# Kernel optimization log

Hardware: AMD Instinct MI355X
Metric: run time of the kernel (lower is better)

The kernel has to match this reference:

```python
import jax, jax.numpy as jnp
import numpy as np

B, T, L = 512, 1024, 48


def setup_inputs() -> dict:
    key = jax.random.key(0)
    k_e, k_tr, k_st, k_en = jax.random.split(key, 4)
    emissions = jax.random.normal(k_e, (B, T, L), dtype=jnp.float32)
    mask = jnp.ones((B, T), dtype=bool)  # unused by the original decode body
    transitions = jax.random.normal(k_tr, (L, L), dtype=jnp.float32) * 0.1
    start_transitions = jax.random.normal(k_st, (L,), dtype=jnp.float32) * 0.1
    end_transitions = jax.random.normal(k_en, (L,), dtype=jnp.float32) * 0.1
    return {
        "emissions": emissions,
        "mask": mask,
        "transitions": transitions,
        "start_transitions": start_transitions,
        "end_transitions": end_transitions,
    }


def reference(emissions, mask, transitions, start_transitions, end_transitions):
    # Viterbi forward (max-plus recurrence) over time, vectorized over batch.
    v0 = start_transitions[None, :] + emissions[:, 0]  # [B, L]

    def step(v, e_t):
        # scores[b, i, j] = v[b, i] + transitions[i, j]
        scores = v[:, :, None] + transitions[None, :, :]  # [B, L, L]
        best = jnp.max(scores, axis=1)                    # [B, L]
        bp = jnp.argmax(scores, axis=1).astype(jnp.int32)  # [B, L] best prev tag
        return best + e_t, bp

    em_rest = jnp.moveaxis(emissions[:, 1:], 1, 0)  # [T-1, B, L]
    v_final, bps = jax.lax.scan(step, v0, em_rest)  # bps: [T-1, B, L]
    v_final = v_final + end_transitions[None, :]
    best_last = jnp.argmax(v_final, axis=1).astype(jnp.int32)  # [B]

    # Backtrack: bps[t] maps tag at time t+1 -> best tag at time t.
    def back(tag, bp):
        prev = jnp.take_along_axis(bp, tag[:, None], axis=1)[:, 0]  # [B]
        return prev, prev

    _, tags_0_to_Tm2 = jax.lax.scan(back, best_last, bps, reverse=True)  # [T-1, B]
    paths = jnp.concatenate([tags_0_to_Tm2, best_last[None, :]], axis=0)  # [T, B]
    return paths.T  # [B, T] decoded tag sequences
```

## Files before the change

kernel.cpp:

```cpp
#include <hip/hip_runtime.h>
#include <math.h>

#define BB 512
#define TT 1024
#define LL 48

__device__ __forceinline__ float readlane_f(float v, int lane) {
    return __int_as_float(__builtin_amdgcn_readlane(__float_as_int(v), lane));
}

__device__ __forceinline__ void argmax48(const float* s, float& bestv, int& besti) {
    float val[24];
    int   idx[24];
#pragma unroll
    for (int k = 0; k < 24; ++k) {
        bool c = s[2 * k + 1] > s[2 * k];
        val[k] = c ? s[2 * k + 1] : s[2 * k];
        idx[k] = c ? 2 * k + 1 : 2 * k;
    }
#pragma unroll
    for (int k = 0; k < 12; ++k) {
        bool c = val[2 * k + 1] > val[2 * k];
        val[k] = c ? val[2 * k + 1] : val[2 * k];
        idx[k] = c ? idx[2 * k + 1] : idx[2 * k];
    }
#pragma unroll
    for (int k = 0; k < 6; ++k) {
        bool c = val[2 * k + 1] > val[2 * k];
        val[k] = c ? val[2 * k + 1] : val[2 * k];
        idx[k] = c ? idx[2 * k + 1] : idx[2 * k];
    }
#pragma unroll
    for (int k = 0; k < 3; ++k) {
        bool c = val[2 * k + 1] > val[2 * k];
        val[k] = c ? val[2 * k + 1] : val[2 * k];
        idx[k] = c ? idx[2 * k + 1] : idx[2 * k];
    }
    bool c01 = val[1] > val[0];
    float bv = c01 ? val[1] : val[0];
    int   bi = c01 ? idx[1] : idx[0];
    bool c2 = val[2] > bv;
    bestv = c2 ? val[2] : bv;
    besti = c2 ? idx[2] : bi;
}

__global__ __launch_bounds__(64) void viterbi_kernel(
    const float* __restrict__ emissions,
    const float* __restrict__ transitions,
    const float* __restrict__ start_tr,
    const float* __restrict__ end_tr,
    int* __restrict__ out)
{
    __shared__ unsigned char bp[(TT - 1) * LL];

    const int b = blockIdx.x;
    const int j = threadIdx.x;
    const int jc = (j < LL) ? j : (LL - 1);

    float tc[LL];
#pragma unroll
    for (int i = 0; i < LL; ++i)
        tc[i] = transitions[i * LL + jc];

    const float* em = emissions + (size_t)b * TT * LL;

    float v = start_tr[jc] + em[jc];

    float e1 = em[1 * LL + jc];
    float e2 = em[2 * LL + jc];

#pragma unroll 3
    for (int t = 1; t < TT; ++t) {
        int tn = t + 2; if (tn >= TT) tn = TT - 1;
        float e3 = em[(size_t)tn * LL + jc];

        float s[LL];
#pragma unroll
        for (int i = 0; i < LL; ++i)
            s[i] = readlane_f(v, i) + tc[i];

        float best; int arg;
        argmax48(s, best, arg);

        v = best + e1;
        bp[(t - 1) * LL + jc] = (unsigned char)arg;

        e1 = e2; e2 = e3;
    }

    v += end_tr[jc];

    float sf[LL];
#pragma unroll
    for (int i = 0; i < LL; ++i)
        sf[i] = readlane_f(v, i);

    float bestv; int tag;
    argmax48(sf, bestv, tag);

    int* ob = out + (size_t)b * TT;
    if (j == 0) ob[TT - 1] = tag;

    __syncthreads();

    for (int hi = TT - 2; hi >= 0; hi -= 32) {
        int lo = hi - 31; if (lo < 0) lo = 0;
        int n = hi - lo + 1;

        unsigned int row[32];
#pragma unroll
        for (int k = 0; k < 32; ++k)
            row[k] = (unsigned int)bp[(lo + k) * LL + jc];

        int outv = 0;
#pragma unroll
        for (int k = 31; k >= 0; --k) {
            if (k < n) {
                tag = __builtin_amdgcn_readlane((int)row[k], tag);
                outv = (j == k) ? tag : outv;
            }
        }
        if (j < n) ob[lo + j] = outv;
    }
}

extern "C" void kernel_launch(void* const* d_in, const int* in_sizes, int n_in,
                              void* d_out, int out_size, void* d_ws, size_t ws_size,
                              hipStream_t stream) {
    const float* emissions   = (const float*)d_in[0];
    const float* transitions = (const float*)d_in[2];
    const float* start_tr    = (const float*)d_in[3];
    const float* end_tr      = (const float*)d_in[4];
    int* out = (int*)d_out;

    viterbi_kernel<<<dim3(BB), dim3(64), 0, stream>>>(
        emissions, transitions, start_tr, end_tr, out);
}
```

Before: 582.4 us.

## Split the Viterbi max-plus reduction across four wavefronts with LDS combine

Each block now runs four wavefronts instead of one. Each wavefront computes a partial max/argmax over 12 of the 48 previous tags. The partial results are packed as value/index pairs into a double-buffered LDS array, and every wave then merges the four candidates after a block barrier. The goal is to cut the serial readlane-and-compare chain per timestep, which dominates this latency-bound recurrence. The cost is an LDS round trip and a __syncthreads on every step, plus four times as many threads holding redundant state. Only wave 0 writes backpointers and runs the backtrack.

```diff
diff --git a/kernel.cpp b/kernel.cpp
--- a/kernel.cpp
+++ b/kernel.cpp
@@ -4,6 +4,8 @@
 #define BB 512
 #define TT 1024
 #define LL 48
+#define NW 4
+#define IW 12
 
 __device__ __forceinline__ float readlane_f(float v, int lane) {
     return __int_as_float(__builtin_amdgcn_readlane(__float_as_int(v), lane));
@@ -44,7 +46,7 @@
     besti = c2 ? idx[2] : bi;
 }
 
-__global__ __launch_bounds__(64) void viterbi_kernel(
+__global__ __launch_bounds__(256) void viterbi_kernel(
     const float* __restrict__ emissions,
     const float* __restrict__ transitions,
     const float* __restrict__ start_tr,
@@ -52,15 +54,19 @@
     int* __restrict__ out)
 {
     __shared__ unsigned char bp[(TT - 1) * LL];
+    __shared__ unsigned long long cb[2][NW * LL];
 
-    const int b = blockIdx.x;
-    const int j = threadIdx.x;
-    const int jc = (j < LL) ? j : (LL - 1);
+    const int b   = blockIdx.x;
+    const int tid = threadIdx.x;
+    const int w   = tid >> 6;
+    const int j   = tid & 63;
+    const int jc  = (j < LL) ? j : (LL - 1);
+    const int ibase = w * IW;
 
-    float tc[LL];
+    float tc[IW];
 #pragma unroll
-    for (int i = 0; i < LL; ++i)
-        tc[i] = transitions[i * LL + jc];
+    for (int k = 0; k < IW; ++k)
+        tc[k] = transitions[(ibase + k) * LL + jc];
 
     const float* em = emissions + (size_t)b * TT * LL;
 
@@ -74,19 +80,62 @@
         int tn = t + 2; if (tn >= TT) tn = TT - 1;
         float e3 = em[(size_t)tn * LL + jc];
 
-        float s[LL];
+        float s[IW];
 #pragma unroll
-        for (int i = 0; i < LL; ++i)
-            s[i] = readlane_f(v, i) + tc[i];
+        for (int k = 0; k < IW; ++k)
+            s[k] = readlane_f(v, ibase + k) + tc[k];
 
-        float best; int arg;
-        argmax48(s, best, arg);
+        float val[6]; int idx[6];
+#pragma unroll
+        for (int k = 0; k < 6; ++k) {
+            bool c = s[2 * k + 1] > s[2 * k];
+            val[k] = c ? s[2 * k + 1] : s[2 * k];
+            idx[k] = ibase + (c ? 2 * k + 1 : 2 * k);
+        }
+#pragma unroll
+        for (int k = 0; k < 3; ++k) {
+            bool c = val[2 * k + 1] > val[2 * k];
+            val[k] = c ? val[2 * k + 1] : val[2 * k];
+            idx[k] = c ? idx[2 * k + 1] : idx[2 * k];
+        }
+        bool c01 = val[1] > val[0];
+        float pv = c01 ? val[1] : val[0];
+        int   pa = c01 ? idx[1] : idx[0];
+        bool c2 = val[2] > pv;
+        pv = c2 ? val[2] : pv;
+        pa = c2 ? idx[2] : pa;
+
+        const int p = t & 1;
+        cb[p][w * LL + jc] =
+            ((unsigned long long)(unsigned)pa << 32) | (unsigned)__float_as_uint(pv);
+
+        __syncthreads();
+
+        float V0, V1, V2, V3; int A0, A1, A2, A3;
+        {
+            unsigned long long q0 = cb[p][0 * LL + jc];
+            unsigned long long q1 = cb[p][1 * LL + jc];
+            unsigned long long q2 = cb[p][2 * LL + jc];
+            unsigned long long q3 = cb[p][3 * LL + jc];
+            V0 = __uint_as_float((unsigned)q0); A0 = (int)(q0 >> 32);
+            V1 = __uint_as_float((unsigned)q1); A1 = (int)(q1 >> 32);
+            V2 = __uint_as_float((unsigned)q2); A2 = (int)(q2 >> 32);
+            V3 = __uint_as_float((unsigned)q3); A3 = (int)(q3 >> 32);
+        }
+        bool ca = V1 > V0;  float va = ca ? V1 : V0;  int aa = ca ? A1 : A0;
+        bool cbb = V3 > V2; float vb = cbb ? V3 : V2; int ab = cbb ? A3 : A2;
+        bool cf = vb > va;
+        float best = cf ? vb : va;
+        int   arg  = cf ? ab : aa;
 
         v = best + e1;
-        bp[(t - 1) * LL + jc] = (unsigned char)arg;
+        if (w == 0)
+            bp[(t - 1) * LL + jc] = (unsigned char)arg;
 
         e1 = e2; e2 = e3;
     }
+
+    if (w != 0) return;
 
     v += end_tr[jc];
 
@@ -100,8 +149,6 @@
 
     int* ob = out + (size_t)b * TT;
     if (j == 0) ob[TT - 1] = tag;
-
-    __syncthreads();
 
     for (int hi = TT - 2; hi >= 0; hi -= 32) {
         int lo = hi - 31; if (lo < 0) lo = 0;
@@ -133,6 +180,6 @@
     const float* end_tr      = (const float*)d_in[4];
     int* out = (int*)d_out;
 
-    viterbi_kernel<<<dim3(BB), dim3(64), 0, stream>>>(
+    viterbi_kernel<<<dim3(BB), dim3(256), 0, stream>>>(
         emissions, transitions, start_tr, end_tr, out);
 }
```

Result: slower. 708.5 us (+21.7%).

## Split Viterbi into max-only producer wave and argmax consumer wave

Applied to the files above, without the earlier changes.

The block grows to two wavefronts. Wave 0 runs the serial recurrence using only fmax reductions, which are cheaper than a tracked argmax. It publishes v and best per step into a 32-slot LDS ring. Wave 1 recovers the argmax by equality matching against best, then writes backpointers and does the backtrack, synchronising through volatile LDS counters with s_sleep spin-waits. This takes the index tracking off the latency-critical recurrence, at the cost of LDS traffic, spin-wait overhead, and the risk of ties or ordering issues in the hand-rolled synchronisation.

```diff
diff --git a/kernel.cpp b/kernel.cpp
--- a/kernel.cpp
+++ b/kernel.cpp
@@ -4,9 +4,17 @@
 #define BB 512
 #define TT 1024
 #define LL 48
+#define DD 32
 
 __device__ __forceinline__ float readlane_f(float v, int lane) {
     return __int_as_float(__builtin_amdgcn_readlane(__float_as_int(v), lane));
+}
+
+__device__ __forceinline__ void lds_fence() {
+    asm volatile("s_waitcnt lgkmcnt(0)" ::: "memory");
+}
+__device__ __forceinline__ void nap() {
+    asm volatile("s_sleep 1");
 }
 
 __device__ __forceinline__ void argmax48(const float* s, float& bestv, int& besti) {
@@ -44,7 +52,7 @@
     besti = c2 ? idx[2] : bi;
 }
 
-__global__ __launch_bounds__(64) void viterbi_kernel(
+__global__ __launch_bounds__(128) void viterbi_kernel(
     const float* __restrict__ emissions,
     const float* __restrict__ transitions,
     const float* __restrict__ start_tr,
@@ -52,75 +60,144 @@
     int* __restrict__ out)
 {
     __shared__ unsigned char bp[(TT - 1) * LL];
-
-    const int b = blockIdx.x;
-    const int j = threadIdx.x;
-    const int jc = (j < LL) ? j : (LL - 1);
+    __shared__ __align__(16) float vring[DD][LL];
+    __shared__ __align__(16) float bring[DD][LL];
+    __shared__ int a_cnt, b_cnt, tag_word;
+
+    const int b   = blockIdx.x;
+    const int tid = threadIdx.x;
+    const int w   = tid >> 6;
+    const int j   = tid & 63;
+    const int jc  = (j < LL) ? j : (LL - 1);
+
+    if (tid == 0) { a_cnt = 0; b_cnt = 0; }
+    __syncthreads();
+
+    volatile int* pa = &a_cnt;
+    volatile int* pb = &b_cnt;
 
     float tc[LL];
 #pragma unroll
     for (int i = 0; i < LL; ++i)
         tc[i] = transitions[i * LL + jc];
 
-    const float* em = emissions + (size_t)b * TT * LL;
-
-    float v = start_tr[jc] + em[jc];
-
-    float e1 = em[1 * LL + jc];
-    float e2 = em[2 * LL + jc];
-
-#pragma unroll 3
-    for (int t = 1; t < TT; ++t) {
-        int tn = t + 2; if (tn >= TT) tn = TT - 1;
-        float e3 = em[(size_t)tn * LL + jc];
-
-        float s[LL];
+    int* ob = out + (size_t)b * TT;
+
+    if (w == 0) {
+        const float* em = emissions + (size_t)b * TT * LL;
+        float v = start_tr[jc] + em[jc];
+        float e1 = em[1 * LL + jc];
+        float e2 = em[2 * LL + jc];
+
+#pragma unroll 2
+        for (int t = 1; t < TT; ++t) {
+            if ((t & 7) == 1) {
+                while (*pb < t - 25) nap();
+            }
+            int tn = t + 2; if (tn >= TT) tn = TT - 1;
+            float e3 = em[(size_t)tn * LL + jc];
+
+            const int slot = t & (DD - 1);
+            *(volatile float*)&vring[slot][jc] = v;
+
+            float s[LL];
+#pragma unroll
+            for (int i = 0; i < LL; ++i)
+                s[i] = readlane_f(v, i) + tc[i];
+
+            float m1[16];
+#pragma unroll
+            for (int k = 0; k < 16; ++k)
+                m1[k] = fmaxf(fmaxf(s[3 * k], s[3 * k + 1]), s[3 * k + 2]);
+            float m2[6];
+#pragma unroll
+            for (int k = 0; k < 5; ++k)
+                m2[k] = fmaxf(fmaxf(m1[3 * k], m1[3 * k + 1]), m1[3 * k + 2]);
+            m2[5] = m1[15];
+            float m3a = fmaxf(fmaxf(m2[0], m2[1]), m2[2]);
+            float m3b = fmaxf(fmaxf(m2[3], m2[4]), m2[5]);
+            float best = fmaxf(m3a, m3b);
+
+            *(volatile float*)&bring[slot][jc] = best;
+            lds_fence();
+            if (j == 0) *pa = t;
+
+            v = best + e1;
+            e1 = e2; e2 = e3;
+        }
+
+        v += end_tr[jc];
+        float sf[LL];
 #pragma unroll
         for (int i = 0; i < LL; ++i)
-            s[i] = readlane_f(v, i) + tc[i];
-
-        float best; int arg;
-        argmax48(s, best, arg);
-
-        v = best + e1;
-        bp[(t - 1) * LL + jc] = (unsigned char)arg;
-
-        e1 = e2; e2 = e3;
-    }
-
-    v += end_tr[jc];
-
-    float sf[LL];
-#pragma unroll
-    for (int i = 0; i < LL; ++i)
-        sf[i] = readlane_f(v, i);
-
-    float bestv; int tag;
-    argmax48(sf, bestv, tag);
-
-    int* ob = out + (size_t)b * TT;
-    if (j == 0) ob[TT - 1] = tag;
-
-    __syncthreads();
-
-    for (int hi = TT - 2; hi >= 0; hi -= 32) {
-        int lo = hi - 31; if (lo < 0) lo = 0;
-        int n = hi - lo + 1;
-
-        unsigned int row[32];
-#pragma unroll
-        for (int k = 0; k < 32; ++k)
-            row[k] = (unsigned int)bp[(lo + k) * LL + jc];
-
-        int outv = 0;
-#pragma unroll
-        for (int k = 31; k >= 0; --k) {
-            if (k < n) {
-                tag = __builtin_amdgcn_readlane((int)row[k], tag);
-                outv = (j == k) ? tag : outv;
-            }
-        }
-        if (j < n) ob[lo + j] = outv;
+            sf[i] = readlane_f(v, i);
+        float bestv; int tag;
+        argmax48(sf, bestv, tag);
+        if (j == 0) {
+            ob[TT - 1] = tag;
+            *(volatile int*)&tag_word = tag;
+        }
+        lds_fence();
+        if (j == 0) *pa = TT;
+    } else {
+        for (int t = 1; t < TT; ++t) {
+            while (*pa < t) nap();
+            lds_fence();
+
+            const int slot = t & (DD - 1);
+            const float4* vp = (const float4*)&vring[slot][0];
+            float vb[LL];
+#pragma unroll
+            for (int k = 0; k < 12; ++k) {
+                float4 q = vp[k];
+                vb[4 * k + 0] = q.x; vb[4 * k + 1] = q.y;
+                vb[4 * k + 2] = q.z; vb[4 * k + 3] = q.w;
+            }
+            float best = bring[slot][jc];
+
+            float s[LL];
+#pragma unroll
+            for (int i = 0; i < LL; ++i)
+                s[i] = vb[i] + tc[i];
+
+            int i0 = 63, i1 = 63, i2 = 63, i3 = 63;
+#pragma unroll
+            for (int k = 11; k >= 0; --k) {
+                if (s[k]      == best) i0 = k;
+                if (s[12 + k] == best) i1 = 12 + k;
+                if (s[24 + k] == best) i2 = 24 + k;
+                if (s[36 + k] == best) i3 = 36 + k;
+            }
+            int arg = min(min(i0, i1), min(i2, i3));
+
+            bp[(t - 1) * LL + jc] = (unsigned char)arg;
+
+            if (((t & 7) == 0) && j == 0) *pb = t;
+        }
+
+        while (*pa < TT) nap();
+        lds_fence();
+        int tag = *(volatile int*)&tag_word;
+
+        for (int hi = TT - 2; hi >= 0; hi -= 32) {
+            int lo = hi - 31; if (lo < 0) lo = 0;
+            int n = hi - lo + 1;
+
+            unsigned int row[32];
+#pragma unroll
+            for (int k = 0; k < 32; ++k)
+                row[k] = (unsigned int)bp[(lo + k) * LL + jc];
+
+            int outv = 0;
+#pragma unroll
+            for (int k = 31; k >= 0; --k) {
+                if (k < n) {
+                    tag = __builtin_amdgcn_readlane((int)row[k], tag);
+                    outv = (j == k) ? tag : outv;
+                }
+            }
+            if (j < n) ob[lo + j] = outv;
+        }
     }
 }
 
@@ -133,6 +210,6 @@
     const float* end_tr      = (const float*)d_in[4];
     int* out = (int*)d_out;
 
-    viterbi_kernel<<<dim3(BB), dim3(64), 0, stream>>>(
+    viterbi_kernel<<<dim3(BB), dim3(128), 0, stream>>>(
         emissions, transitions, start_tr, end_tr, out);
 }
```

New measurement: 960.0 us. 64.8% more time.

## Broadcast Viterbi scores through LDS and split max from argmax search

Applied to the files above, without the earlier changes.

Each step now writes the per-lane score into a shared buffer and reads it back as twelve float4 loads, replacing 48 cross-lane readlane broadcasts. The fused compare-and-select argmax tree becomes a max-only reduction using three-way fmax. A separate equality scan then recovers the first matching index, which keeps the first-index tie-breaking. The LDS write and read now sit on the serial per-step dependency chain, which may add latency, and the barrier before backtracking is removed because the block is a single wavefront.

```diff
diff --git a/kernel.cpp b/kernel.cpp
--- a/kernel.cpp
+++ b/kernel.cpp
@@ -52,9 +52,10 @@
     int* __restrict__ out)
 {
     __shared__ unsigned char bp[(TT - 1) * LL];
+    __shared__ __align__(16) float vbuf[64];
 
-    const int b = blockIdx.x;
-    const int j = threadIdx.x;
+    const int b  = blockIdx.x;
+    const int j  = threadIdx.x;
     const int jc = (j < LL) ? j : (LL - 1);
 
     float tc[LL];
@@ -74,34 +75,57 @@
         int tn = t + 2; if (tn >= TT) tn = TT - 1;
         float e3 = em[(size_t)tn * LL + jc];
 
+        vbuf[j] = v;
         float s[LL];
+        const float4* vp = (const float4*)vbuf;
 #pragma unroll
-        for (int i = 0; i < LL; ++i)
-            s[i] = readlane_f(v, i) + tc[i];
+        for (int k = 0; k < 12; ++k) {
+            float4 q = vp[k];
+            s[4 * k + 0] = q.x + tc[4 * k + 0];
+            s[4 * k + 1] = q.y + tc[4 * k + 1];
+            s[4 * k + 2] = q.z + tc[4 * k + 2];
+            s[4 * k + 3] = q.w + tc[4 * k + 3];
+        }
 
-        float best; int arg;
-        argmax48(s, best, arg);
+        float m1[16];
+#pragma unroll
+        for (int k = 0; k < 16; ++k)
+            m1[k] = fmaxf(fmaxf(s[3 * k], s[3 * k + 1]), s[3 * k + 2]);
+        float m2[6];
+#pragma unroll
+        for (int k = 0; k < 5; ++k)
+            m2[k] = fmaxf(fmaxf(m1[3 * k], m1[3 * k + 1]), m1[3 * k + 2]);
+        m2[5] = m1[15];
+        float best = fmaxf(fmaxf(fmaxf(m2[0], m2[1]), m2[2]),
+                           fmaxf(fmaxf(m2[3], m2[4]), m2[5]));
 
         v = best + e1;
+
+        int i0 = 63, i1 = 63, i2 = 63, i3 = 63;
+#pragma unroll
+        for (int k = 11; k >= 0; --k) {
+            if (s[k]      == best) i0 = k;
+            if (s[12 + k] == best) i1 = 12 + k;
+            if (s[24 + k] == best) i2 = 24 + k;
+            if (s[36 + k] == best) i3 = 36 + k;
+        }
+        int arg = min(min(i0, i1), min(i2, i3));
+
         bp[(t - 1) * LL + jc] = (unsigned char)arg;
 
         e1 = e2; e2 = e3;
     }
 
     v += end_tr[jc];
-
     float sf[LL];
 #pragma unroll
     for (int i = 0; i < LL; ++i)
         sf[i] = readlane_f(v, i);
-
     float bestv; int tag;
     argmax48(sf, bestv, tag);
 
     int* ob = out + (size_t)b * TT;
     if (j == 0) ob[TT - 1] = tag;
-
-    __syncthreads();
 
     for (int hi = TT - 2; hi >= 0; hi -= 32) {
         int lo = hi - 31; if (lo < 0) lo = 0;
```

Result: slower. 628.3 us (+7.9%).
